# Performance work log

Measured on AMD Instinct MI355X. Metric: run time of the kernel, lower is better.

Reference implementation:

```python
import jax, jax.numpy as jnp
import numpy as np

SEQ_LEN = 16384
D = 2048
K = 50          # tagset size
START = 48
STOP = 49
NEG = -10000.0


def setup_inputs() -> dict:
    key = jax.random.key(0)
    k1, k2, k3, k4 = jax.random.split(key, 4)
    input_var = jax.random.normal(k1, (SEQ_LEN, D), jnp.float32)
    tags = jax.random.randint(k2, (SEQ_LEN,), 0, 48, dtype=jnp.int32)  # real tags only
    W = jax.random.normal(k3, (K, D), jnp.float32) * 0.02              # hidden2tag weight
    b = jnp.zeros((K,), jnp.float32)                                   # hidden2tag bias
    transitions = jax.random.normal(k4, (K, K), jnp.float32) * 0.1
    # match the torch init: no transition into START, none out of STOP
    transitions = transitions.at[START, :].set(NEG).at[:, STOP].set(NEG)
    return {"input_var": input_var, "tags": tags, "W": W, "b": b, "transitions": transitions}


def reference(input_var, tags, W, b, transitions):
    # dropout in eval mode == identity (faithful deterministic forward)
    feats = input_var @ W.T + b  # [T, K] emission scores

    # --- CRF forward algorithm (log partition) ---
    alpha0 = jnp.full((K,), NEG, jnp.float32).at[START].set(0.0)

    def step(alpha, feat):
        # tag_var[i, j] = alpha[j] + transitions[i, j] + feat[i]
        s = alpha[None, :] + transitions           # [K, K]
        m = jnp.max(s, axis=1)                     # stable log-sum-exp
        alpha_new = feat + m + jnp.log(jnp.sum(jnp.exp(s - m[:, None]), axis=1))
        return alpha_new, None

    alpha, _ = jax.lax.scan(step, alpha0, feats)
    term = alpha + transitions[STOP]
    mt = jnp.max(term)
    forward_score = mt + jnp.log(jnp.sum(jnp.exp(term - mt)))

    # --- gold path score ---
    pad_start = jnp.concatenate([jnp.array([START], dtype=tags.dtype), tags])
    pad_stop = jnp.concatenate([tags, jnp.array([STOP], dtype=tags.dtype)])
    gold = (jnp.sum(transitions[pad_stop, pad_start])
            + jnp.sum(feats[jnp.arange(SEQ_LEN), tags]))

    return forward_score - gold
```

## Files before the change

kernel.cpp:

```cpp
#include <hip/hip_runtime.h>

typedef unsigned short u16;
typedef unsigned int u32;
typedef __bf16 b16x8 __attribute__((ext_vector_type(8)));
typedef float f32x16 __attribute__((ext_vector_type(16)));

#define SEQ   16384
#define DM    2048
#define KT    50
#define NST   48
#define NSP   49

__device__ __forceinline__ int perm64(int g){
  int q = (g>>2)&3;
  return (q==1 || q==2) ? (g^12) : g;
}
__device__ __forceinline__ u16 bfb(float f){
  __bf16 b = (__bf16)f;
  return __builtin_bit_cast(u16, b);
}
__device__ __forceinline__ int pk2(float a, float b){
  return (int)((u32)bfb(a) | ((u32)bfb(b) << 16));
}
__device__ __forceinline__ b16x8 cast8(int4 v){ return __builtin_bit_cast(b16x8, v); }

__device__ __forceinline__ f32x16 mfma_(b16x8 a, b16x8 b, f32x16 c){
  return __builtin_amdgcn_mfma_f32_32x32x16_bf16(a, b, c, 0, 0, 0);
}

__device__ __forceinline__ void mm64(const b16x8 A[2][4], const b16x8 B[4][2], f32x16 acc[2][2]){
#pragma unroll
  for (int mi=0; mi<2; ++mi)
#pragma unroll
    for (int ni=0; ni<2; ++ni){
      f32x16 a;
#pragma unroll
      for (int q=0;q<16;q++) a[q] = 0.0f;
#pragma unroll
      for (int kt=0; kt<4; ++kt) a = mfma_(A[mi][kt], B[kt][ni], a);
      acc[mi][ni] = a;
    }
}

__device__ __forceinline__ void repack(const f32x16 acc[2][2], b16x8 B[4][2]){
#pragma unroll
  for (int kb=0; kb<4; ++kb){
    const int mi = kb>>1, t = kb&1;
#pragma unroll
    for (int ni=0; ni<2; ++ni){
      int4 dw;
      dw.x = pk2(acc[mi][ni][8*t+0], acc[mi][ni][8*t+1]);
      dw.y = pk2(acc[mi][ni][8*t+2], acc[mi][ni][8*t+3]);
      dw.z = pk2(acc[mi][ni][8*t+4], acc[mi][ni][8*t+5]);
      dw.w = pk2(acc[mi][ni][8*t+6], acc[mi][ni][8*t+7]);
      B[kb][ni] = cast8(dw);
    }
  }
}
__device__ __forceinline__ void repack_s(const f32x16 acc[2][2], b16x8 B[4][2], float s){
#pragma unroll
  for (int kb=0; kb<4; ++kb){
    const int mi = kb>>1, t = kb&1;
#pragma unroll
    for (int ni=0; ni<2; ++ni){
      int4 dw;
      dw.x = pk2(acc[mi][ni][8*t+0]*s, acc[mi][ni][8*t+1]*s);
      dw.y = pk2(acc[mi][ni][8*t+2]*s, acc[mi][ni][8*t+3]*s);
      dw.z = pk2(acc[mi][ni][8*t+4]*s, acc[mi][ni][8*t+5]*s);
      dw.w = pk2(acc[mi][ni][8*t+6]*s, acc[mi][ni][8*t+7]*s);
      B[kb][ni] = cast8(dw);
    }
  }
}

template<int PERM>
__device__ __forceinline__ void ident_frags(b16x8 B[4][2], int lane){
  const int h = lane>>5, j0 = lane&31;
#pragma unroll
  for (int kt=0; kt<4; ++kt)
#pragma unroll
    for (int ni=0; ni<2; ++ni){
      const int col = j0 + 32*ni;
      int d[4];
#pragma unroll
      for (int dd=0; dd<4; ++dd){
        int r0 = 16*kt + 8*h + 2*dd, r1 = r0 + 1;
        int p0 = PERM ? perm64(r0) : r0;
        int p1 = PERM ? perm64(r1) : r1;
        d[dd] = (int)((p0==col ? 0x3F80u : 0u) | ((p1==col ? 0x3F80u : 0u) << 16));
      }
      int4 v; v.x=d[0]; v.y=d[1]; v.z=d[2]; v.w=d[3];
      B[kt][ni] = cast8(v);
    }
}

__device__ __forceinline__ float acc_wave_max(const f32x16 acc[2][2]){
  float m = 0.0f;
#pragma unroll
  for (int mi=0;mi<2;mi++)
#pragma unroll
    for (int ni=0;ni<2;ni++)
#pragma unroll
      for (int q=0;q<16;q++) m = fmaxf(m, acc[mi][ni][q]);
#pragma unroll
  for (int o=32;o>=1;o>>=1) m = fmaxf(m, __shfl_xor(m, o, 64));
  return m;
}

template<int PROW>
__device__ __forceinline__ void store_mat_lds(u16* mat, const f32x16 acc[2][2], float inv, int lane){
  const int h = lane>>5, j0 = lane&31;
#pragma unroll
  for (int mi=0;mi<2;mi++)
#pragma unroll
    for (int ni=0;ni<2;ni++)
#pragma unroll
      for (int r=0;r<16;r++){
        int gp = 32*mi + (r&3) + 8*(r>>2) + 4*h;
        int a = PROW ? perm64(gp) : gp;
        int b = perm64(32*ni + j0);
        mat[a*64 + (b ^ ((a&7)<<3))] = bfb(acc[mi][ni][r]*inv);
      }
}
template<int PROW>
__device__ __forceinline__ void store_mat_glob(u16* mat, const f32x16 acc[2][2], float inv, int lane){
  const int h = lane>>5, j0 = lane&31;
#pragma unroll
  for (int mi=0;mi<2;mi++)
#pragma unroll
    for (int ni=0;ni<2;ni++)
#pragma unroll
      for (int r=0;r<16;r++){
        int gp = 32*mi + (r&3) + 8*(r>>2) + 4*h;
        int a = PROW ? perm64(gp) : gp;
        int b = perm64(32*ni + j0);
        mat[a*64 + b] = bfb(acc[mi][ni][r]*inv);
      }
}
__device__ __forceinline__ void load_afrag_lds(const u16* mat, b16x8 A[2][4], int lane){
  const int h = lane>>5, i0 = lane&31;
#pragma unroll
  for (int mi=0;mi<2;mi++)
#pragma unroll
    for (int kt=0;kt<4;kt++){
      int i = 32*mi + i0;
      int cb = (16*kt + 8*h) ^ ((i&7)<<3);
      A[mi][kt] = cast8(*(const int4*)(mat + i*64 + cb));
    }
}
__device__ __forceinline__ void load_afrag_glob(const u16* mat, b16x8 A[2][4], int lane){
  const int h = lane>>5, i0 = lane&31;
#pragma unroll
  for (int mi=0;mi<2;mi++)
#pragma unroll
    for (int kt=0;kt<4;kt++){
      int i = 32*mi + i0;
      A[mi][kt] = cast8(*(const int4*)(mat + i*64 + 16*kt + 8*h));
    }
}

__global__ __launch_bounds__(512, 2) void k_fused(const float* __restrict__ in,
      const int* __restrict__ tags, const float* __restrict__ W,
      const float* __restrict__ bias, const float* __restrict__ T,
      float* __restrict__ gpart, u16* __restrict__ M1, float* __restrict__ S1){
  __shared__ __align__(16) char smem[131072];
  u16* const bA = (u16*)smem;
  u16* const bB = (u16*)(smem + 32768);
  __shared__ float logs[8];
  const int t = threadIdx.x;
  const int w = t>>6, lane = t&63;
  const int j0 = lane&31, h = lane>>5;
  const int rh = w&1, ch = (w>>1)&1, kq = (w>>2)&1;
  const int row0 = blockIdx.x*64;
  const int aswz = (j0&7)<<3;

  float rA[2][8], rB[2][8];
  f32x16 acc;
#pragma unroll
  for (int q=0;q<16;q++) acc[q]=0.f;

#define LOADCHUNK(kc)                                                       \
  { _Pragma("unroll")                                                       \
    for (int i=0;i<2;i++){                                                  \
      int g=(i<<9)+t; int r=g>>4, c8=g&15;                                  \
      const float* p = in + (size_t)(row0+r)*DM + (kc)*128 + c8*8;          \
      float4 f0=*(const float4*)p, f1=*(const float4*)(p+4);                \
      rA[i][0]=f0.x; rA[i][1]=f0.y; rA[i][2]=f0.z; rA[i][3]=f0.w;           \
      rA[i][4]=f1.x; rA[i][5]=f1.y; rA[i][6]=f1.z; rA[i][7]=f1.w;           \
      if (r < KT){                                                          \
        const float* q2 = W + (size_t)r*DM + (kc)*128 + c8*8;               \
        float4 g0=*(const float4*)q2, g1=*(const float4*)(q2+4);            \
        rB[i][0]=g0.x; rB[i][1]=g0.y; rB[i][2]=g0.z; rB[i][3]=g0.w;         \
        rB[i][4]=g1.x; rB[i][5]=g1.y; rB[i][6]=g1.z; rB[i][7]=g1.w;         \
      } else {                                                              \
        _Pragma("unroll") for (int z=0;z<8;z++) rB[i][z]=0.f;               \
      }                                                                     \
    } }
#define WRITECHUNK(d)                                                       \
  { _Pragma("unroll")                                                       \
    for (int i=0;i<2;i++){                                                  \
      int g=(i<<9)+t; int r=g>>4, c8=g&15;                                  \
      int off = r*128 + ((c8*8) ^ ((r&7)<<3));                              \
      int4 da; da.x=pk2(rA[i][0],rA[i][1]); da.y=pk2(rA[i][2],rA[i][3]);    \
      da.z=pk2(rA[i][4],rA[i][5]); da.w=pk2(rA[i][6],rA[i][7]);             \
      *(int4*)(bA + (d)*8192 + off) = da;                                   \
      int4 db; db.x=pk2(rB[i][0],rB[i][1]); db.y=pk2(rB[i][2],rB[i][3]);    \
      db.z=pk2(rB[i][4],rB[i][5]); db.w=pk2(rB[i][6],rB[i][7]);             \
      *(int4*)(bB + (d)*8192 + off) = db;                                   \
    } }

  LOADCHUNK(0); WRITECHUNK(0);
  __syncthreads();
  for (int kc=0; kc<16; ++kc){
    const int d = kc & 1;
    if (kc < 15) LOADCHUNK(kc+1);
    const u16* Arow = bA + d*8192 + (32*rh + j0)*128;
    const u16* Brow = bB + d*8192 + (32*ch + j0)*128;
#pragma unroll
    for (int kk=0;kk<4;kk++){
      const int kt = kq*4 + kk;
      b16x8 aF = cast8(*(const int4*)(Arow + ((kt*16 + h*8) ^ aswz)));
      b16x8 bF = cast8(*(const int4*)(Brow + ((kt*16 + h*8) ^ aswz)));
      acc = mfma_(aF, bF, acc);
    }
    if (kc < 15) WRITECHUNK(d^1);
    __syncthreads();
  }
#undef LOADCHUNK
#undef WRITECHUNK

  float* planes = (float*)smem;
  float* tile   = (float*)(smem + 32768);
  float* mrow   = (float*)(smem + 49664);
  u16*   mats   = (u16*)  (smem + 65536);
#pragma unroll
  for (int r=0;r<16;r++){
    int gp = (r&3) + 8*(r>>2) + 4*h;
    planes[kq*4096 + (32*rh + gp)*64 + 32*ch + j0] = acc[r];
  }
  float E32[2][4][8];
  {
    const int pr = perm64(j0);
#pragma unroll
    for (int mi=0;mi<2;mi++){
      const int prow = 32*mi + pr;
#pragma unroll
      for (int kt=0;kt<4;kt++)
#pragma unroll
        for (int j=0;j<8;j++){
          const int c = 16*kt + 8*h + j;
          E32[mi][kt][j] = (prow < KT && c < KT) ? __expf(T[prow*50 + c]) : 0.f;
        }
    }
  }
  __syncthreads();
  for (int cidx = t; cidx < 4096; cidx += 512){
    int g = cidx>>6, c = cidx&63;
    float v = planes[cidx] + planes[4096 + cidx];
    tile[g*66 + c] = (c<KT) ? (v + bias[c]) : -1e4f;
  }
  __syncthreads();
  if (t < 64){
    int g = t;
    float mx = -1e30f;
    for (int c=0;c<KT;c++) mx = fmaxf(mx, tile[g*66+c]);
    mrow[g] = mx;
    int tt = row0 + g;
    int s1 = tags[tt];
    int s0 = (tt==0) ? NST : tags[tt-1];
    float part = (tile[g*66 + s1] - mx) + T[s1*50 + s0];
    if (tt == SEQ-1) part += T[NSP*50 + s1];
#pragma unroll
    for (int o=32;o>=1;o>>=1) part += __shfl_xor(part, o, 64);
    if (t==0) gpart[blockIdx.x] = part;
  }
  __syncthreads();

  {
    b16x8 Bf[4][2];
    ident_frags<0>(Bf, lane);
    const int pr = perm64(j0);
    const int tr0 = w*8;
    float x0 = tile[tr0*66 + pr]      - mrow[tr0];
    float x1 = tile[tr0*66 + 32 + pr] - mrow[tr0];
    f32x16 sacc[2][2];
#pragma unroll 1
    for (int s=0;s<8;s++){
      float u0 = __expf(x0), u1 = __expf(x1);
      if (s<7){
        x0 = tile[(tr0+s+1)*66 + pr]      - mrow[tr0+s+1];
        x1 = tile[(tr0+s+1)*66 + 32 + pr] - mrow[tr0+s+1];
      }
      b16x8 Af[2][4];
#pragma unroll
      for (int mi=0;mi<2;mi++){
        const float uu = mi ? u1 : u0;
#pragma unroll
        for (int kt=0;kt<4;kt++){
          int4 dw;
          dw.x = pk2(uu*E32[mi][kt][0], uu*E32[mi][kt][1]);
          dw.y = pk2(uu*E32[mi][kt][2], uu*E32[mi][kt][3]);
          dw.z = pk2(uu*E32[mi][kt][4], uu*E32[mi][kt][5]);
          dw.w = pk2(uu*E32[mi][kt][6], uu*E32[mi][kt][7]);
          Af[mi][kt] = cast8(dw);
        }
      }
      mm64(Af, Bf, sacc);
      repack(sacc, Bf);
    }
    float m = acc_wave_max(sacc);
    store_mat_lds<1>(mats + w*4096, sacc, 1.0f/m, lane);
    if (lane==0) logs[w] = __logf(m);
  }
  __syncthreads();
  if (w==0){
    float slog = logs[0]+logs[1]+logs[2]+logs[3]+logs[4]+logs[5]+logs[6]+logs[7];
    b16x8 Bc[4][2]; ident_frags<1>(Bc, lane);
    f32x16 a2[2][2];
#pragma unroll 1
    for (int m8=0;m8<8;m8++){
      b16x8 Am[2][4];
      load_afrag_lds(mats + m8*4096, Am, lane);
      mm64(Am, Bc, a2);
      repack(a2, Bc);
    }
    float m2 = acc_wave_max(a2);
    slog += __logf(m2);
    store_mat_glob<0>(M1 + (size_t)blockIdx.x*4096, a2, 1.0f/m2, lane);
    if (lane==0) S1[blockIdx.x] = slog;
  }
}

__global__ __launch_bounds__(512, 2) void k_final(const u16* __restrict__ M1,
      const float* __restrict__ S1, const float* __restrict__ T,
      const float* __restrict__ gpart, float* __restrict__ out){
  const int t = threadIdx.x;
  const int w = t>>6, lane = t&63;
  const int h = lane>>5;
  __shared__ __align__(16) u16 mats[8][4096];
  __shared__ float logs[8];
  __shared__ float alpha[64];

  {
    const int base = w*32;
    b16x8 Bc[4][2]; ident_frags<1>(Bc, lane);
    f32x16 a2[2][2];
    float sl = 0.f;
    b16x8 A0[2][4], A1[2][4], A2[2][4], A3[2][4];
    load_afrag_glob(M1 + (size_t)(base+0)*4096, A0, lane);
    load_afrag_glob(M1 + (size_t)(base+1)*4096, A1, lane);
    load_afrag_glob(M1 + (size_t)(base+2)*4096, A2, lane);
#pragma unroll 1
    for (int mm=0; mm<32; mm++){
      if (mm<29) load_afrag_glob(M1 + (size_t)(base+mm+3)*4096, A3, lane);
      sl += S1[base+mm];
      mm64(A0, Bc, a2);
      if (mm!=31 && (mm&7)==7){
        float mx = acc_wave_max(a2);
        sl += __logf(mx);
        repack_s(a2, Bc, 1.0f/mx);
      } else {
        repack(a2, Bc);
      }
#pragma unroll
      for (int mi=0;mi<2;mi++)
#pragma unroll
        for (int kt=0;kt<4;kt++){
          A0[mi][kt]=A1[mi][kt]; A1[mi][kt]=A2[mi][kt]; A2[mi][kt]=A3[mi][kt];
        }
    }
    float mx = acc_wave_max(a2);
    sl += __logf(mx);
    store_mat_lds<0>(mats[w], a2, 1.0f/mx, lane);
    if (lane==0) logs[w] = sl;
  }
  __syncthreads();
  if (w==0){
    b16x8 Bc[4][2]; ident_frags<1>(Bc, lane);
    f32x16 a2[2][2];
#pragma unroll 1
    for (int m8=0;m8<8;m8++){
      b16x8 Am[2][4];
      load_afrag_lds(mats[m8], Am, lane);
      mm64(Am, Bc, a2);
      repack(a2, Bc);
    }
    float slog = logs[0]+logs[1]+logs[2]+logs[3]+logs[4]+logs[5]+logs[6]+logs[7];
    if ((lane&31)==16){
#pragma unroll
      for (int mi=0;mi<2;mi++)
#pragma unroll
        for (int r=0;r<16;r++){
          int gp = 32*mi + (r&3) + 8*(r>>2) + 4*h;
          alpha[gp] = a2[mi][1][r];
        }
    }
    float gold = gpart[lane] + gpart[lane+64] + gpart[lane+128] + gpart[lane+192];
#pragma unroll
    for (int o=32;o>=1;o>>=1) gold += __shfl_xor(gold, o, 64);
    float a = alpha[lane];
    float term = (lane < KT && a > 0.f) ? (__logf(a) + slog + T[NSP*50 + lane]) : -1e30f;
    float tm = term;
#pragma unroll
    for (int o=32;o>=1;o>>=1) tm = fmaxf(tm, __shfl_xor(tm, o, 64));
    float e = __expf(term - tm);
#pragma unroll
    for (int o=32;o>=1;o>>=1) e += __shfl_xor(e, o, 64);
    if (lane==0) out[0] = (tm + __logf(e)) - gold;
  }
}

extern "C" void kernel_launch(void* const* d_in, const int* in_sizes, int n_in,
                              void* d_out, int out_size, void* d_ws, size_t ws_size,
                              hipStream_t stream) {
  (void)in_sizes; (void)n_in; (void)out_size; (void)ws_size;
  const float* input = (const float*)d_in[0];
  const int*   tags  = (const int*)  d_in[1];
  const float* W     = (const float*)d_in[2];
  const float* bias  = (const float*)d_in[3];
  const float* T     = (const float*)d_in[4];

  char* ws = (char*)d_ws;
  float* gpart = (float*)(ws + 0);
  u16*   M1    = (u16*)  (ws + 1024);
  float* S1    = (float*)(ws + 2098176);

  k_fused<<<256, 512, 0, stream>>>(input, tags, W, bias, T, gpart, M1, S1);
  k_final<<<1,   512, 0, stream>>>(M1, S1, T, gpart, (float*)d_out);
}
```

Before: 121.6 us.

## Tree-reduce per-wave CRF matrix products and shrink fused kernel LDS

The fused kernel now combines the eight per-wave 64x64 transfer-matrix products with a log-depth pairwise tree reduction across waves, replacing a serial chain of eight matmuls on wave 0. The exponentials of the emission rows are precomputed into an LDS table, so the per-step exp sits outside the dependent matmul loop. LDS drops from 128 KB to about 65 KB, which could allow two blocks per CU. The tree needs extra barriers and changes the multiplication order and the row/column permutation templates, so the layout conventions must stay consistent between the two kernels.

```diff
diff --git a/kernel.cpp b/kernel.cpp
--- a/kernel.cpp
+++ b/kernel.cpp
@@ -107,7 +107,7 @@
   return m;
 }
 
-template<int PROW>
+template<int PROW, int PCOL>
 __device__ __forceinline__ void store_mat_lds(u16* mat, const f32x16 acc[2][2], float inv, int lane){
   const int h = lane>>5, j0 = lane&31;
 #pragma unroll
@@ -118,11 +118,12 @@
       for (int r=0;r<16;r++){
         int gp = 32*mi + (r&3) + 8*(r>>2) + 4*h;
         int a = PROW ? perm64(gp) : gp;
-        int b = perm64(32*ni + j0);
+        int cc = 32*ni + j0;
+        int b = PCOL ? perm64(cc) : cc;
         mat[a*64 + (b ^ ((a&7)<<3))] = bfb(acc[mi][ni][r]*inv);
       }
 }
-template<int PROW>
+template<int PROW, int PCOL>
 __device__ __forceinline__ void store_mat_glob(u16* mat, const f32x16 acc[2][2], float inv, int lane){
   const int h = lane>>5, j0 = lane&31;
 #pragma unroll
@@ -133,7 +134,8 @@
       for (int r=0;r<16;r++){
         int gp = 32*mi + (r&3) + 8*(r>>2) + 4*h;
         int a = PROW ? perm64(gp) : gp;
-        int b = perm64(32*ni + j0);
+        int cc = 32*ni + j0;
+        int b = PCOL ? perm64(cc) : cc;
         mat[a*64 + b] = bfb(acc[mi][ni][r]*inv);
       }
 }
@@ -163,10 +165,10 @@
       const int* __restrict__ tags, const float* __restrict__ W,
       const float* __restrict__ bias, const float* __restrict__ T,
       float* __restrict__ gpart, u16* __restrict__ M1, float* __restrict__ S1){
-  __shared__ __align__(16) char smem[131072];
+  __shared__ __align__(16) char smem[66560];
   u16* const bA = (u16*)smem;
   u16* const bB = (u16*)(smem + 32768);
-  __shared__ float logs[8];
+  __shared__ float logs_l[8];
   const int t = threadIdx.x;
   const int w = t>>6, lane = t&63;
   const int j0 = lane&31, h = lane>>5;
@@ -232,7 +234,8 @@
   float* planes = (float*)smem;
   float* tile   = (float*)(smem + 32768);
   float* mrow   = (float*)(smem + 49664);
-  u16*   mats   = (u16*)  (smem + 65536);
+  float* ue     = (float*)(smem + 50176);
+  u16*   tmats  = (u16*)  smem;
 #pragma unroll
   for (int r=0;r<16;r++){
     int gp = (r&3) + 8*(r>>2) + 4*h;
@@ -275,22 +278,22 @@
     if (t==0) gpart[blockIdx.x] = part;
   }
   __syncthreads();
-
+  for (int cidx = t; cidx < 4096; cidx += 512){
+    int g = cidx>>6, c = cidx&63;
+    ue[cidx] = __expf(tile[g*66 + c] - mrow[g]);
+  }
+  __syncthreads();
+
+  b16x8 Bf[4][2];
+  ident_frags<0>(Bf, lane);
+  f32x16 sacc[2][2];
   {
-    b16x8 Bf[4][2];
-    ident_frags<0>(Bf, lane);
     const int pr = perm64(j0);
     const int tr0 = w*8;
-    float x0 = tile[tr0*66 + pr]      - mrow[tr0];
-    float x1 = tile[tr0*66 + 32 + pr] - mrow[tr0];
-    f32x16 sacc[2][2];
 #pragma unroll 1
     for (int s=0;s<8;s++){
-      float u0 = __expf(x0), u1 = __expf(x1);
-      if (s<7){
-        x0 = tile[(tr0+s+1)*66 + pr]      - mrow[tr0+s+1];
-        x1 = tile[(tr0+s+1)*66 + 32 + pr] - mrow[tr0+s+1];
-      }
+      float u0 = ue[(tr0+s)*64 + pr];
+      float u1 = ue[(tr0+s)*64 + 32 + pr];
       b16x8 Af[2][4];
 #pragma unroll
       for (int mi=0;mi<2;mi++){
@@ -308,26 +311,36 @@
       mm64(Af, Bf, sacc);
       repack(sacc, Bf);
     }
-    float m = acc_wave_max(sacc);
-    store_mat_lds<1>(mats + w*4096, sacc, 1.0f/m, lane);
-    if (lane==0) logs[w] = __logf(m);
-  }
-  __syncthreads();
+  }
+  float m = acc_wave_max(sacc);
+  float sl = __logf(m);
+  float inv = 1.0f/m;
+  int active = 1;
+#pragma unroll 1
+  for (int l=0; l<3; ++l){
+    const int storer = active && ((w>>l)&1);
+    if (active && lane==0) logs_l[w] = sl;
+    if (storer){
+      store_mat_lds<0,0>(tmats + (w>>(l+1))*4096, sacc, inv, lane);
+    } else if (active){
+      repack_s(sacc, Bf, inv);
+    }
+    __syncthreads();
+    if (active && !storer){
+      b16x8 Am[2][4];
+      load_afrag_lds(tmats + (w>>(l+1))*4096, Am, lane);
+      mm64(Am, Bf, sacc);
+      sl += logs_l[w + (1<<l)];
+      m = acc_wave_max(sacc);
+      sl += __logf(m);
+      inv = 1.0f/m;
+    }
+    if (storer) active = 0;
+    __syncthreads();
+  }
   if (w==0){
-    float slog = logs[0]+logs[1]+logs[2]+logs[3]+logs[4]+logs[5]+logs[6]+logs[7];
-    b16x8 Bc[4][2]; ident_frags<1>(Bc, lane);
-    f32x16 a2[2][2];
-#pragma unroll 1
-    for (int m8=0;m8<8;m8++){
-      b16x8 Am[2][4];
-      load_afrag_lds(mats + m8*4096, Am, lane);
-      mm64(Am, Bc, a2);
-      repack(a2, Bc);
-    }
-    float m2 = acc_wave_max(a2);
-    slog += __logf(m2);
-    store_mat_glob<0>(M1 + (size_t)blockIdx.x*4096, a2, 1.0f/m2, lane);
-    if (lane==0) S1[blockIdx.x] = slog;
+    store_mat_glob<1,0>(M1 + (size_t)blockIdx.x*4096, sacc, inv, lane);
+    if (lane==0) S1[blockIdx.x] = sl;
   }
 }
 
@@ -371,7 +384,7 @@
     }
     float mx = acc_wave_max(a2);
     sl += __logf(mx);
-    store_mat_lds<0>(mats[w], a2, 1.0f/mx, lane);
+    store_mat_lds<0,1>(mats[w], a2, 1.0f/mx, lane);
     if (lane==0) logs[w] = sl;
   }
   __syncthreads();
```

Result: no change. 120.4 us (-1.0%).
